# Optimization experiments

Measured on AMD Instinct MI355X. Metric: run time of the kernel, lower is better.

## Reference

```python
import jax, jax.numpy as jnp
import numpy as np
import math

B, N, HW, D, H = 4, 1024, 4096, 512, 8
DK = D // H
EPS = 0.1


def setup_inputs() -> dict:
    key = jax.random.key(0)
    ks = jax.random.split(key, 12)
    s = 1.0 / math.sqrt(D)
    query = jax.random.normal(ks[0], (B, N, D), dtype=jnp.float32)
    key_t = jax.random.normal(ks[1], (B, HW, D), dtype=jnp.float32)
    value = jax.random.normal(ks[2], (B, HW, D), dtype=jnp.float32)
    # 2D spatial positions of the feature map in [0,1]^2
    x_tilde = jax.random.uniform(ks[3], (HW, 2), dtype=jnp.float32)
    # predicted positions per query: close to x_tilde so each row has unmasked keys
    x_hat = x_tilde[None, :, :] + 0.1 * jax.random.normal(ks[4], (N, HW, 2), dtype=jnp.float32)
    Wq = jax.random.normal(ks[5], (D, D), dtype=jnp.float32) * s
    Wk = jax.random.normal(ks[6], (D, D), dtype=jnp.float32) * s
    Wv = jax.random.normal(ks[7], (D, D), dtype=jnp.float32) * s
    Wo = jax.random.normal(ks[8], (D, D), dtype=jnp.float32) * s
    bq = jnp.zeros((D,), jnp.float32)
    bk = jnp.zeros((D,), jnp.float32)
    bv = jnp.zeros((D,), jnp.float32)
    bo = jnp.zeros((D,), jnp.float32)
    return {"query": query, "key": key_t, "value": value,
            "x_tilde": x_tilde, "x_hat": x_hat,
            "Wq": Wq, "bq": bq, "Wk": Wk, "bk": bk,
            "Wv": Wv, "bv": bv, "Wo": Wo, "bo": bo}


def reference(query, key, value, x_tilde, x_hat, Wq, bq, Wk, bk, Wv, bv, Wo, bo):
    b, n, d = query.shape
    hw = key.shape[1]
    # nn.Linear: x @ W^T + b
    Q = (query @ Wq.T + bq).reshape(b, n, H, DK).transpose(0, 2, 1, 3)   # [B,H,N,DK]
    K = (key @ Wk.T + bk).reshape(b, hw, H, DK).transpose(0, 2, 1, 3)    # [B,H,HW,DK]
    V = (value @ Wv.T + bv).reshape(b, hw, H, DK).transpose(0, 2, 1, 3)  # [B,H,HW,DK]
    scores = jnp.einsum('bhnd,bhmd->bhnm', Q, K) / math.sqrt(DK)         # [B,H,N,HW]
    # geometric mask: 0 where ||x_tilde_j - x_hat_ij|| < eps else -inf
    dist = jnp.linalg.norm(x_tilde[None, :, :] - x_hat, axis=-1)         # [N,HW]
    m_geo = jnp.where(dist < EPS, 0.0, -jnp.inf).astype(scores.dtype)
    scores = scores + m_geo[None, None, :, :]
    attn = jax.nn.softmax(scores, axis=-1)                               # [B,H,N,HW]
    # dropout is identity in eval mode
    ctx = jnp.einsum('bhnm,bhmd->bhnd', attn, V)                         # [B,H,N,DK]
    ctx = ctx.transpose(0, 2, 1, 3).reshape(b, n, d)
    out = ctx @ Wo.T + bo
    return (out, attn)
```

## Files before the change

kernel.cpp:

```cpp
#include <hip/hip_runtime.h>
#include <math.h>

typedef _Float16 h8 __attribute__((ext_vector_type(8)));
typedef _Float16 h4 __attribute__((ext_vector_type(4)));
typedef float    f4 __attribute__((ext_vector_type(4)));

#define NQ    1024
#define HWK   4096
#define DM    512
#define NH    8
#define DKH   64

__device__ inline h8 cvt_h8(const float* __restrict__ p) {
    const f4* q = (const f4*)p;
    f4 a = q[0], b = q[1];
    h8 r;
    r[0] = (_Float16)a[0]; r[1] = (_Float16)a[1];
    r[2] = (_Float16)a[2]; r[3] = (_Float16)a[3];
    r[4] = (_Float16)b[0]; r[5] = (_Float16)b[1];
    r[6] = (_Float16)b[2]; r[7] = (_Float16)b[3];
    return r;
}

__global__ __launch_bounds__(256)
void mask_kernel(const float* __restrict__ x_tilde, const float* __restrict__ x_hat,
                 _Float16* __restrict__ maskT)
{
    __shared__ _Float16 T[64][72];
    int t  = threadIdx.x;
    int jl = t & 63;
    int iw = t >> 6;
    int j0 = blockIdx.x * 64;
    int i0 = blockIdx.y * 64;

    float xt0 = x_tilde[(j0 + jl) * 2 + 0];
    float xt1 = x_tilde[(j0 + jl) * 2 + 1];

    for (int ii = iw; ii < 64; ii += 4) {
        size_t idx = ((size_t)(i0 + ii) * HWK + j0 + jl) * 2;
        float h0 = x_hat[idx + 0];
        float h1 = x_hat[idx + 1];
        float dx = xt0 - h0, dy = xt1 - h1;
        float d2 = __fadd_rn(__fmul_rn(dx, dx), __fmul_rn(dy, dy));
        float dist = __fsqrt_rn(d2);
        T[ii][jl] = (dist < 0.1f) ? (_Float16)0.0f : (_Float16)(-__builtin_inff());
    }
    __syncthreads();
    int il = t & 63;
    for (int jj = iw; jj < 64; jj += 4) {
        maskT[(size_t)(j0 + jj) * NQ + i0 + il] = T[il][jj];
    }
}

__global__ __launch_bounds__(256)
void proj_qk(const float* __restrict__ X, const float* __restrict__ W,
             const float* __restrict__ bias, _Float16* __restrict__ out,
             int nlog2, float scale)
{
    int tid = threadIdx.x;
    int w = tid >> 6, lane = tid & 63, q = lane >> 4, c = lane & 15;
    int wr = blockIdx.x * 128 + (w >> 1) * 64;
    int wc = blockIdx.y * 128 + (w & 1) * 64;

    f4 acc[4][4];
    const f4 fz = {0.f, 0.f, 0.f, 0.f};
#pragma unroll
    for (int i = 0; i < 4; i++)
#pragma unroll
        for (int j = 0; j < 4; j++) acc[i][j] = fz;

    for (int k0 = 0; k0 < DM; k0 += 32) {
        h8 af[4], bf[4];
#pragma unroll
        for (int i = 0; i < 4; i++)
            af[i] = cvt_h8(X + (size_t)(wr + i * 16 + c) * DM + k0 + q * 8);
#pragma unroll
        for (int j = 0; j < 4; j++)
            bf[j] = cvt_h8(W + (size_t)(wc + j * 16 + c) * DM + k0 + q * 8);
#pragma unroll
        for (int i = 0; i < 4; i++)
#pragma unroll
            for (int j = 0; j < 4; j++)
                acc[i][j] = __builtin_amdgcn_mfma_f32_16x16x32_f16(af[i], bf[j], acc[i][j], 0, 0, 0);
    }

    int nmask = (1 << nlog2) - 1;
#pragma unroll
    for (int j = 0; j < 4; j++) {
        int ncol = wc + j * 16 + c;
        float bb = bias[ncol];
        int hh = ncol >> 6, dk = ncol & 63;
#pragma unroll
        for (int i = 0; i < 4; i++) {
#pragma unroll
            for (int r = 0; r < 4; r++) {
                int m = wr + i * 16 + q * 4 + r;
                int b = m >> nlog2, n = m & nmask;
                float v = (acc[i][j][r] + bb) * scale;
                out[((((size_t)(b * NH + hh)) << nlog2) + n) * DKH + dk] = (_Float16)v;
            }
        }
    }
}

__global__ __launch_bounds__(256)
void proj_v(const float* __restrict__ V, const float* __restrict__ W,
            const float* __restrict__ bias, _Float16* __restrict__ out)
{
    int tid = threadIdx.x;
    int w = tid >> 6, lane = tid & 63, q = lane >> 4, c = lane & 15;
    int wr = blockIdx.x * 128 + (w >> 1) * 64;
    int wc = blockIdx.y * 128 + (w & 1) * 64;

    f4 acc[4][4];
    const f4 fz = {0.f, 0.f, 0.f, 0.f};
#pragma unroll
    for (int i = 0; i < 4; i++)
#pragma unroll
        for (int j = 0; j < 4; j++) acc[i][j] = fz;

    for (int k0 = 0; k0 < DM; k0 += 32) {
        h8 af[4], bf[4];
#pragma unroll
        for (int i = 0; i < 4; i++)
            af[i] = cvt_h8(W + (size_t)(wr + i * 16 + c) * DM + k0 + q * 8);
#pragma unroll
        for (int j = 0; j < 4; j++)
            bf[j] = cvt_h8(V + (size_t)(wc + j * 16 + c) * DM + k0 + q * 8);
#pragma unroll
        for (int i = 0; i < 4; i++)
#pragma unroll
            for (int j = 0; j < 4; j++)
                acc[i][j] = __builtin_amdgcn_mfma_f32_16x16x32_f16(af[i], bf[j], acc[i][j], 0, 0, 0);
    }

#pragma unroll
    for (int i = 0; i < 4; i++) {
#pragma unroll
        for (int r = 0; r < 4; r++) {
            int f = wr + i * 16 + q * 4 + r;
            float bb = bias[f];
            int hh = f >> 6, dk = f & 63;
#pragma unroll
            for (int j = 0; j < 4; j++) {
                int col = wc + j * 16 + c;
                int b = col >> 12, hw = col & 4095;
                out[((size_t)(b * NH + hh) * DKH + dk) * HWK + hw] =
                    (_Float16)(acc[i][j][r] + bb);
            }
        }
    }
}

__global__ __launch_bounds__(256)
void proj_o(const _Float16* __restrict__ C, const float* __restrict__ W,
            const float* __restrict__ bias, float* __restrict__ out)
{
    int tid = threadIdx.x;
    int w = tid >> 6, lane = tid & 63, q = lane >> 4, c = lane & 15;
    int wr = blockIdx.x * 128 + (w >> 1) * 64;
    int wc = blockIdx.y * 128 + (w & 1) * 64;

    f4 acc[4][4];
    const f4 fz = {0.f, 0.f, 0.f, 0.f};
#pragma unroll
    for (int i = 0; i < 4; i++)
#pragma unroll
        for (int j = 0; j < 4; j++) acc[i][j] = fz;

    for (int k0 = 0; k0 < DM; k0 += 32) {
        h8 af[4], bf[4];
#pragma unroll
        for (int i = 0; i < 4; i++)
            af[i] = *(const h8*)(C + (size_t)(wr + i * 16 + c) * DM + k0 + q * 8);
#pragma unroll
        for (int j = 0; j < 4; j++)
            bf[j] = cvt_h8(W + (size_t)(wc + j * 16 + c) * DM + k0 + q * 8);
#pragma unroll
        for (int i = 0; i < 4; i++)
#pragma unroll
            for (int j = 0; j < 4; j++)
                acc[i][j] = __builtin_amdgcn_mfma_f32_16x16x32_f16(af[i], bf[j], acc[i][j], 0, 0, 0);
    }

#pragma unroll
    for (int j = 0; j < 4; j++) {
        int ncol = wc + j * 16 + c;
        float bb = bias[ncol];
#pragma unroll
        for (int i = 0; i < 4; i++) {
#pragma unroll
            for (int r = 0; r < 4; r++) {
                int m = wr + i * 16 + q * 4 + r;
                out[(size_t)m * DM + ncol] = acc[i][j][r] + bb;
            }
        }
    }
}

__global__ __launch_bounds__(256)
void attn_kernel(const _Float16* __restrict__ Qh, const _Float16* __restrict__ Kh,
                 const _Float16* __restrict__ Vt, const _Float16* __restrict__ maskT,
                 float* __restrict__ attn_out, _Float16* __restrict__ ctx_h)
{
    __shared__ union SmU {
        _Float16 P[4][64][72];
        float    C[64][68];
    } sm;
    __shared__ float red[4][64];
    __shared__ float invl[64];

    int tid = threadIdx.x;
    int w = tid >> 6, lane = tid & 63, q = lane >> 4, c = lane & 15;
    int bh = blockIdx.x >> 4;
    int n0 = (blockIdx.x & 15) * 64;
    int b = bh >> 3, h = bh & 7;

    const _Float16* Qb = Qh + ((size_t)bh * NQ + n0) * DKH;
    const _Float16* Kb = Kh + (size_t)bh * HWK * DKH;
    const _Float16* Vb = Vt + (size_t)bh * DKH * HWK;
    float* attn_b = attn_out + ((size_t)bh * NQ + n0) * HWK;

    h8 qa[4][2];
#pragma unroll
    for (int i = 0; i < 4; i++)
#pragma unroll
        for (int ks = 0; ks < 2; ks++)
            qa[i][ks] = *(const h8*)(Qb + (size_t)(i * 16 + c) * DKH + ks * 32 + q * 8);

    float lsum[4][4];
#pragma unroll
    for (int i = 0; i < 4; i++)
#pragma unroll
        for (int r = 0; r < 4; r++) lsum[i][r] = 0.f;

    for (int it = 0; it < 16; ++it) {
        int m0 = it * 256 + w * 64;
        h8 kb[4][2];
#pragma unroll
        for (int j = 0; j < 4; j++)
#pragma unroll
            for (int ks = 0; ks < 2; ks++)
                kb[j][ks] = *(const h8*)(Kb + (size_t)(m0 + j * 16 + c) * DKH + ks * 32 + q * 8);
#pragma unroll
        for (int i = 0; i < 4; i++) {
#pragma unroll
            for (int j = 0; j < 4; j++) {
                f4 acc = {0.f, 0.f, 0.f, 0.f};
                acc = __builtin_amdgcn_mfma_f32_16x16x32_f16(qa[i][0], kb[j][0], acc, 0, 0, 0);
                acc = __builtin_amdgcn_mfma_f32_16x16x32_f16(qa[i][1], kb[j][1], acc, 0, 0, 0);
                h4 mk = *(const h4*)(maskT + (size_t)(m0 + j * 16 + c) * NQ + n0 + i * 16 + q * 4);
#pragma unroll
                for (int r = 0; r < 4; r++)
                    lsum[i][r] += __expf(acc[r] + (float)mk[r]);
            }
        }
    }

#pragma unroll
    for (int i = 0; i < 4; i++) {
#pragma unroll
        for (int r = 0; r < 4; r++) {
            float s = lsum[i][r];
            s += __shfl_xor(s, 1);
            s += __shfl_xor(s, 2);
            s += __shfl_xor(s, 4);
            s += __shfl_xor(s, 8);
            if (c == 0) red[w][i * 16 + q * 4 + r] = s;
        }
    }
    __syncthreads();
    if (tid < 64)
        invl[tid] = 1.0f / (red[0][tid] + red[1][tid] + red[2][tid] + red[3][tid]);
    __syncthreads();

    f4 cacc[4][4];
    const f4 fz = {0.f, 0.f, 0.f, 0.f};
#pragma unroll
    for (int i = 0; i < 4; i++)
#pragma unroll
        for (int jd = 0; jd < 4; jd++) cacc[i][jd] = fz;

    for (int it = 0; it < 16; ++it) {
        int m0 = it * 256 + w * 64;
        h8 kb[4][2];
#pragma unroll
        for (int j = 0; j < 4; j++)
#pragma unroll
            for (int ks = 0; ks < 2; ks++)
                kb[j][ks] = *(const h8*)(Kb + (size_t)(m0 + j * 16 + c) * DKH + ks * 32 + q * 8);

#pragma unroll
        for (int i = 0; i < 4; i++) {
#pragma unroll
            for (int j = 0; j < 4; j++) {
                f4 acc = {0.f, 0.f, 0.f, 0.f};
                acc = __builtin_amdgcn_mfma_f32_16x16x32_f16(qa[i][0], kb[j][0], acc, 0, 0, 0);
                acc = __builtin_amdgcn_mfma_f32_16x16x32_f16(qa[i][1], kb[j][1], acc, 0, 0, 0);
                h4 mk = *(const h4*)(maskT + (size_t)(m0 + j * 16 + c) * NQ + n0 + i * 16 + q * 4);
#pragma unroll
                for (int r = 0; r < 4; r++) {
                    float e = __expf(acc[r] + (float)mk[r]);
                    sm.P[w][i * 16 + q * 4 + r][j * 16 + c] = (_Float16)e;
                }
            }
        }
#pragma unroll
        for (int ks = 0; ks < 2; ks++) {
            h8 pa[4], vb[4];
#pragma unroll
            for (int i = 0; i < 4; i++)
                pa[i] = *(const h8*)&sm.P[w][i * 16 + c][ks * 32 + q * 8];
#pragma unroll
            for (int jd = 0; jd < 4; jd++)
                vb[jd] = *(const h8*)(Vb + (size_t)(jd * 16 + c) * HWK + m0 + ks * 32 + q * 8);
#pragma unroll
            for (int i = 0; i < 4; i++)
#pragma unroll
                for (int jd = 0; jd < 4; jd++)
                    cacc[i][jd] = __builtin_amdgcn_mfma_f32_16x16x32_f16(pa[i], vb[jd], cacc[i][jd], 0, 0, 0);
        }
#pragma unroll
        for (int r0 = 0; r0 < 64; r0 += 4) {
            int row = r0 + q;
            h4 pv = *(const h4*)&sm.P[w][row][c * 4];
            float il = invl[row];
            f4 o;
            o[0] = (float)pv[0] * il;
            o[1] = (float)pv[1] * il;
            o[2] = (float)pv[2] * il;
            o[3] = (float)pv[3] * il;
            *(f4*)(attn_b + (size_t)row * HWK + m0 + c * 4) = o;
        }
    }

    __syncthreads();
    for (int idx = tid; idx < 64 * 68; idx += 256)
        (&sm.C[0][0])[idx] = 0.f;
    __syncthreads();
#pragma unroll
    for (int i = 0; i < 4; i++)
#pragma unroll
        for (int jd = 0; jd < 4; jd++)
#pragma unroll
            for (int r = 0; r < 4; r++)
                atomicAdd(&sm.C[i * 16 + q * 4 + r][jd * 16 + c], cacc[i][jd][r]);
    __syncthreads();

    _Float16* ctx_b = ctx_h + ((size_t)b * NQ + n0) * DM + h * DKH;
    for (int r0 = 0; r0 < 64; r0 += 4) {
        int row = r0 + w;
        int col = tid & 63;
        float v = sm.C[row][col] * invl[row];
        ctx_b[(size_t)row * DM + col] = (_Float16)v;
    }
}

extern "C" void kernel_launch(void* const* d_in, const int* in_sizes, int n_in,
                              void* d_out, int out_size, void* d_ws, size_t ws_size,
                              hipStream_t stream)
{
    const float* query   = (const float*)d_in[0];
    const float* key     = (const float*)d_in[1];
    const float* value   = (const float*)d_in[2];
    const float* x_tilde = (const float*)d_in[3];
    const float* x_hat   = (const float*)d_in[4];
    const float* Wq = (const float*)d_in[5];
    const float* bq = (const float*)d_in[6];
    const float* Wk = (const float*)d_in[7];
    const float* bk = (const float*)d_in[8];
    const float* Wv = (const float*)d_in[9];
    const float* bv = (const float*)d_in[10];
    const float* Wo = (const float*)d_in[11];
    const float* bo = (const float*)d_in[12];

    char* ws = (char*)d_ws;
    _Float16* Qh    = (_Float16*)(ws);
    _Float16* Kh    = (_Float16*)(ws + ((size_t)4  << 20));
    _Float16* Vt    = (_Float16*)(ws + ((size_t)20 << 20));
    _Float16* ctxh  = (_Float16*)(ws + ((size_t)36 << 20));
    _Float16* maskT = (_Float16*)(ws + ((size_t)40 << 20));

    float* out  = (float*)d_out;
    float* attn = out + (size_t)4 * NQ * DM;

    mask_kernel<<<dim3(HWK / 64, NQ / 64), 256, 0, stream>>>(x_tilde, x_hat, maskT);
    proj_qk<<<dim3(4 * NQ / 128, DM / 128), 256, 0, stream>>>(query, Wq, bq, Qh, 10, 0.125f);
    proj_qk<<<dim3(4 * HWK / 128, DM / 128), 256, 0, stream>>>(key, Wk, bk, Kh, 12, 1.0f);
    proj_v<<<dim3(DM / 128, 4 * HWK / 128), 256, 0, stream>>>(value, Wv, bv, Vt);
    attn_kernel<<<32 * (NQ / 64), 256, 0, stream>>>(Qh, Kh, Vt, maskT, attn, ctxh);
    proj_o<<<dim3(4 * NQ / 128, DM / 128), 256, 0, stream>>>(ctxh, Wo, bo, out);
}
```

Baseline: 1.039 ms.

## Split attention into score/exp kernel and PV kernel with materialized fp16 exp buffer

Replaces the fused two-pass attention kernel, which computed QK^T twice, with one kernel that computes exp(scores+mask) once. That kernel writes the values to an fp16 global buffer and atomically accumulates row sums. A second kernel reads the buffer to do the PV matmul and write the normalized attention output. The mask is now stored untransposed in row order, and the recompute of the score matmul is removed. In exchange it adds a 268MB fp16 write and reads it back twice, plus an extra memset and launch.

Measured after the change: 1.240 ms. 1.19x slower.

```diff
diff --git a/kernel.cpp b/kernel.cpp
--- a/kernel.cpp
+++ b/kernel.cpp
@@ -24,32 +24,19 @@
 
 __global__ __launch_bounds__(256)
 void mask_kernel(const float* __restrict__ x_tilde, const float* __restrict__ x_hat,
-                 _Float16* __restrict__ maskT)
-{
-    __shared__ _Float16 T[64][72];
-    int t  = threadIdx.x;
-    int jl = t & 63;
-    int iw = t >> 6;
-    int j0 = blockIdx.x * 64;
-    int i0 = blockIdx.y * 64;
-
-    float xt0 = x_tilde[(j0 + jl) * 2 + 0];
-    float xt1 = x_tilde[(j0 + jl) * 2 + 1];
-
-    for (int ii = iw; ii < 64; ii += 4) {
-        size_t idx = ((size_t)(i0 + ii) * HWK + j0 + jl) * 2;
-        float h0 = x_hat[idx + 0];
-        float h1 = x_hat[idx + 1];
-        float dx = xt0 - h0, dy = xt1 - h1;
-        float d2 = __fadd_rn(__fmul_rn(dx, dx), __fmul_rn(dy, dy));
-        float dist = __fsqrt_rn(d2);
-        T[ii][jl] = (dist < 0.1f) ? (_Float16)0.0f : (_Float16)(-__builtin_inff());
-    }
-    __syncthreads();
-    int il = t & 63;
-    for (int jj = iw; jj < 64; jj += 4) {
-        maskT[(size_t)(j0 + jj) * NQ + i0 + il] = T[il][jj];
-    }
+                 _Float16* __restrict__ mask)
+{
+    int hw = blockIdx.x * 256 + threadIdx.x;
+    int n  = blockIdx.y;
+    float xt0 = x_tilde[hw * 2 + 0];
+    float xt1 = x_tilde[hw * 2 + 1];
+    size_t idx = ((size_t)n * HWK + hw) * 2;
+    float dx = xt0 - x_hat[idx + 0];
+    float dy = xt1 - x_hat[idx + 1];
+    float d2 = __fadd_rn(__fmul_rn(dx, dx), __fmul_rn(dy, dy));
+    float dist = __fsqrt_rn(d2);
+    mask[(size_t)n * HWK + hw] = (dist < 0.1f) ? (_Float16)0.0f
+                                               : (_Float16)(-__builtin_inff());
 }
 
 __global__ __launch_bounds__(256)
@@ -199,160 +186,147 @@
 }
 
 __global__ __launch_bounds__(256)
-void attn_kernel(const _Float16* __restrict__ Qh, const _Float16* __restrict__ Kh,
-                 const _Float16* __restrict__ Vt, const _Float16* __restrict__ maskT,
-                 float* __restrict__ attn_out, _Float16* __restrict__ ctx_h)
-{
-    __shared__ union SmU {
-        _Float16 P[4][64][72];
-        float    C[64][68];
-    } sm;
+void attn_scores(const _Float16* __restrict__ Qh, const _Float16* __restrict__ Kh,
+                 const _Float16* __restrict__ mask,
+                 _Float16* __restrict__ eBuf, float* __restrict__ lsum_g)
+{
     __shared__ float red[4][64];
-    __shared__ float invl[64];
-
-    int tid = threadIdx.x;
-    int w = tid >> 6, lane = tid & 63, q = lane >> 4, c = lane & 15;
-    int bh = blockIdx.x >> 4;
-    int n0 = (blockIdx.x & 15) * 64;
-    int b = bh >> 3, h = bh & 7;
+    int tid = threadIdx.x;
+    int w = tid >> 6, lane = tid & 63, q = lane >> 4, c = lane & 15;
+    int bx = blockIdx.x;
+    int mt = bx & 3, nt = (bx >> 2) & 15, bh = bx >> 6;
+    int n0 = nt * 64;
 
     const _Float16* Qb = Qh + ((size_t)bh * NQ + n0) * DKH;
     const _Float16* Kb = Kh + (size_t)bh * HWK * DKH;
+    _Float16* eb = eBuf + (size_t)bh * NQ * HWK;
+
+    h8 qb[4][2];
+#pragma unroll
+    for (int j = 0; j < 4; j++)
+#pragma unroll
+        for (int ks = 0; ks < 2; ks++)
+            qb[j][ks] = *(const h8*)(Qb + (size_t)(j * 16 + c) * DKH + ks * 32 + q * 8);
+
+    float lsum[4] = {0.f, 0.f, 0.f, 0.f};
+
+    for (int it = 0; it < 4; ++it) {
+        int m0 = mt * 1024 + w * 256 + it * 64;
+        h8 ka[4][2];
+#pragma unroll
+        for (int i = 0; i < 4; i++)
+#pragma unroll
+            for (int ks = 0; ks < 2; ks++)
+                ka[i][ks] = *(const h8*)(Kb + (size_t)(m0 + i * 16 + c) * DKH + ks * 32 + q * 8);
+
+#pragma unroll
+        for (int i = 0; i < 4; i++) {
+#pragma unroll
+            for (int j = 0; j < 4; j++) {
+                f4 acc = {0.f, 0.f, 0.f, 0.f};
+                acc = __builtin_amdgcn_mfma_f32_16x16x32_f16(ka[i][0], qb[j][0], acc, 0, 0, 0);
+                acc = __builtin_amdgcn_mfma_f32_16x16x32_f16(ka[i][1], qb[j][1], acc, 0, 0, 0);
+                size_t roff = (size_t)(n0 + j * 16 + c) * HWK + m0 + i * 16 + q * 4;
+                h4 mk = *(const h4*)(mask + roff);
+                h4 ev;
+#pragma unroll
+                for (int r = 0; r < 4; r++) {
+                    float e = __expf(acc[r] + (float)mk[r]);
+                    lsum[j] += e;
+                    ev[r] = (_Float16)e;
+                }
+                *(h4*)(eb + roff) = ev;
+            }
+        }
+    }
+
+#pragma unroll
+    for (int j = 0; j < 4; j++) {
+        float s = lsum[j];
+        s += __shfl_xor(s, 16);
+        s += __shfl_xor(s, 32);
+        if (q == 0) red[w][j * 16 + c] = s;
+    }
+    __syncthreads();
+    if (tid < 64)
+        atomicAdd(lsum_g + (size_t)bh * NQ + n0 + tid,
+                  red[0][tid] + red[1][tid] + red[2][tid] + red[3][tid]);
+}
+
+__global__ __launch_bounds__(256)
+void attn_pv(const _Float16* __restrict__ eBuf, const _Float16* __restrict__ Vt,
+             const float* __restrict__ lsum_g,
+             float* __restrict__ attn_out, _Float16* __restrict__ ctx_h)
+{
+    __shared__ float invS[16];
+    __shared__ float Cr[16][68];
+
+    int tid = threadIdx.x;
+    int w = tid >> 6, lane = tid & 63, q = lane >> 4, c = lane & 15;
+    int nt = blockIdx.x & 63, bh = blockIdx.x >> 6;
+    int n0 = nt * 16;
+
+    if (tid < 16) invS[tid] = 1.0f / lsum_g[(size_t)bh * NQ + n0 + tid];
+    for (int idx = tid; idx < 16 * 68; idx += 256) (&Cr[0][0])[idx] = 0.f;
+    __syncthreads();
+
+    const _Float16* eb = eBuf + ((size_t)bh * NQ + n0) * HWK;
     const _Float16* Vb = Vt + (size_t)bh * DKH * HWK;
-    float* attn_b = attn_out + ((size_t)bh * NQ + n0) * HWK;
-
-    h8 qa[4][2];
-#pragma unroll
-    for (int i = 0; i < 4; i++)
-#pragma unroll
-        for (int ks = 0; ks < 2; ks++)
-            qa[i][ks] = *(const h8*)(Qb + (size_t)(i * 16 + c) * DKH + ks * 32 + q * 8);
-
-    float lsum[4][4];
-#pragma unroll
-    for (int i = 0; i < 4; i++)
-#pragma unroll
-        for (int r = 0; r < 4; r++) lsum[i][r] = 0.f;
+    float* ab = attn_out + ((size_t)bh * NQ + n0) * HWK;
+
+    f4 cacc[4];
+    const f4 fz = {0.f, 0.f, 0.f, 0.f};
+#pragma unroll
+    for (int jd = 0; jd < 4; jd++) cacc[jd] = fz;
 
     for (int it = 0; it < 16; ++it) {
         int m0 = it * 256 + w * 64;
-        h8 kb[4][2];
-#pragma unroll
-        for (int j = 0; j < 4; j++)
+        h8 pa[2];
+#pragma unroll
+        for (int ks = 0; ks < 2; ks++)
+            pa[ks] = *(const h8*)(eb + (size_t)c * HWK + m0 + ks * 32 + q * 8);
+        h8 vb[4][2];
+#pragma unroll
+        for (int jd = 0; jd < 4; jd++)
 #pragma unroll
             for (int ks = 0; ks < 2; ks++)
-                kb[j][ks] = *(const h8*)(Kb + (size_t)(m0 + j * 16 + c) * DKH + ks * 32 + q * 8);
-#pragma unroll
-        for (int i = 0; i < 4; i++) {
-#pragma unroll
-            for (int j = 0; j < 4; j++) {
-                f4 acc = {0.f, 0.f, 0.f, 0.f};
-                acc = __builtin_amdgcn_mfma_f32_16x16x32_f16(qa[i][0], kb[j][0], acc, 0, 0, 0);
-                acc = __builtin_amdgcn_mfma_f32_16x16x32_f16(qa[i][1], kb[j][1], acc, 0, 0, 0);
-                h4 mk = *(const h4*)(maskT + (size_t)(m0 + j * 16 + c) * NQ + n0 + i * 16 + q * 4);
-#pragma unroll
-                for (int r = 0; r < 4; r++)
-                    lsum[i][r] += __expf(acc[r] + (float)mk[r]);
-            }
-        }
-    }
-
-#pragma unroll
-    for (int i = 0; i < 4; i++) {
-#pragma unroll
-        for (int r = 0; r < 4; r++) {
-            float s = lsum[i][r];
-            s += __shfl_xor(s, 1);
-            s += __shfl_xor(s, 2);
-            s += __shfl_xor(s, 4);
-            s += __shfl_xor(s, 8);
-            if (c == 0) red[w][i * 16 + q * 4 + r] = s;
-        }
-    }
+                vb[jd][ks] = *(const h8*)(Vb + (size_t)(jd * 16 + c) * HWK + m0 + ks * 32 + q * 8);
+#pragma unroll
+        for (int jd = 0; jd < 4; jd++) {
+            cacc[jd] = __builtin_amdgcn_mfma_f32_16x16x32_f16(pa[0], vb[jd][0], cacc[jd], 0, 0, 0);
+            cacc[jd] = __builtin_amdgcn_mfma_f32_16x16x32_f16(pa[1], vb[jd][1], cacc[jd], 0, 0, 0);
+        }
+#pragma unroll
+        for (int s = 0; s < 2; s++) {
+            int row = s * 8 + (lane >> 3);
+            int mc = (lane & 7) * 8;
+            h8 e8 = *(const h8*)(eb + (size_t)row * HWK + m0 + mc);
+            float il = invS[row];
+            f4 o0, o1;
+            o0[0] = (float)e8[0] * il; o0[1] = (float)e8[1] * il;
+            o0[2] = (float)e8[2] * il; o0[3] = (float)e8[3] * il;
+            o1[0] = (float)e8[4] * il; o1[1] = (float)e8[5] * il;
+            o1[2] = (float)e8[6] * il; o1[3] = (float)e8[7] * il;
+            float* dst = ab + (size_t)row * HWK + m0 + mc;
+            *(f4*)dst = o0;
+            *(f4*)(dst + 4) = o1;
+        }
+    }
+
+#pragma unroll
+    for (int jd = 0; jd < 4; jd++)
+#pragma unroll
+        for (int r = 0; r < 4; r++)
+            atomicAdd(&Cr[q * 4 + r][jd * 16 + c], cacc[jd][r]);
     __syncthreads();
-    if (tid < 64)
-        invl[tid] = 1.0f / (red[0][tid] + red[1][tid] + red[2][tid] + red[3][tid]);
-    __syncthreads();
-
-    f4 cacc[4][4];
-    const f4 fz = {0.f, 0.f, 0.f, 0.f};
-#pragma unroll
-    for (int i = 0; i < 4; i++)
-#pragma unroll
-        for (int jd = 0; jd < 4; jd++) cacc[i][jd] = fz;
-
-    for (int it = 0; it < 16; ++it) {
-        int m0 = it * 256 + w * 64;
-        h8 kb[4][2];
-#pragma unroll
-        for (int j = 0; j < 4; j++)
-#pragma unroll
-            for (int ks = 0; ks < 2; ks++)
-                kb[j][ks] = *(const h8*)(Kb + (size_t)(m0 + j * 16 + c) * DKH + ks * 32 + q * 8);
-
-#pragma unroll
-        for (int i = 0; i < 4; i++) {
-#pragma unroll
-            for (int j = 0; j < 4; j++) {
-                f4 acc = {0.f, 0.f, 0.f, 0.f};
-                acc = __builtin_amdgcn_mfma_f32_16x16x32_f16(qa[i][0], kb[j][0], acc, 0, 0, 0);
-                acc = __builtin_amdgcn_mfma_f32_16x16x32_f16(qa[i][1], kb[j][1], acc, 0, 0, 0);
-                h4 mk = *(const h4*)(maskT + (size_t)(m0 + j * 16 + c) * NQ + n0 + i * 16 + q * 4);
-#pragma unroll
-                for (int r = 0; r < 4; r++) {
-                    float e = __expf(acc[r] + (float)mk[r]);
-                    sm.P[w][i * 16 + q * 4 + r][j * 16 + c] = (_Float16)e;
-                }
-            }
-        }
-#pragma unroll
-        for (int ks = 0; ks < 2; ks++) {
-            h8 pa[4], vb[4];
-#pragma unroll
-            for (int i = 0; i < 4; i++)
-                pa[i] = *(const h8*)&sm.P[w][i * 16 + c][ks * 32 + q * 8];
-#pragma unroll
-            for (int jd = 0; jd < 4; jd++)
-                vb[jd] = *(const h8*)(Vb + (size_t)(jd * 16 + c) * HWK + m0 + ks * 32 + q * 8);
-#pragma unroll
-            for (int i = 0; i < 4; i++)
-#pragma unroll
-                for (int jd = 0; jd < 4; jd++)
-                    cacc[i][jd] = __builtin_amdgcn_mfma_f32_16x16x32_f16(pa[i], vb[jd], cacc[i][jd], 0, 0, 0);
-        }
-#pragma unroll
-        for (int r0 = 0; r0 < 64; r0 += 4) {
-            int row = r0 + q;
-            h4 pv = *(const h4*)&sm.P[w][row][c * 4];
-            float il = invl[row];
-            f4 o;
-            o[0] = (float)pv[0] * il;
-            o[1] = (float)pv[1] * il;
-            o[2] = (float)pv[2] * il;
-            o[3] = (float)pv[3] * il;
-            *(f4*)(attn_b + (size_t)row * HWK + m0 + c * 4) = o;
-        }
-    }
-
-    __syncthreads();
-    for (int idx = tid; idx < 64 * 68; idx += 256)
-        (&sm.C[0][0])[idx] = 0.f;
-    __syncthreads();
-#pragma unroll
-    for (int i = 0; i < 4; i++)
-#pragma unroll
-        for (int jd = 0; jd < 4; jd++)
-#pragma unroll
-            for (int r = 0; r < 4; r++)
-                atomicAdd(&sm.C[i * 16 + q * 4 + r][jd * 16 + c], cacc[i][jd][r]);
-    __syncthreads();
-
-    _Float16* ctx_b = ctx_h + ((size_t)b * NQ + n0) * DM + h * DKH;
-    for (int r0 = 0; r0 < 64; r0 += 4) {
-        int row = r0 + w;
+
+    int b = bh >> 3, h = bh & 7;
+    _Float16* cb = ctx_h + ((size_t)b * NQ + n0) * DM + h * DKH;
+#pragma unroll
+    for (int g = 0; g < 4; g++) {
+        int row = g * 4 + (tid >> 6);
         int col = tid & 63;
-        float v = sm.C[row][col] * invl[row];
-        ctx_b[(size_t)row * DM + col] = (_Float16)v;
+        cb[(size_t)row * DM + col] = (_Float16)(Cr[row][col] * invS[row]);
     }
 }
 
@@ -379,15 +353,20 @@
     _Float16* Kh    = (_Float16*)(ws + ((size_t)4  << 20));
     _Float16* Vt    = (_Float16*)(ws + ((size_t)20 << 20));
     _Float16* ctxh  = (_Float16*)(ws + ((size_t)36 << 20));
-    _Float16* maskT = (_Float16*)(ws + ((size_t)40 << 20));
+    _Float16* mask  = (_Float16*)(ws + ((size_t)40 << 20));
+    float*    lsum  = (float*)   (ws + ((size_t)48 << 20));
+    _Float16* eBuf  = (_Float16*)(ws + ((size_t)52 << 20));
 
     float* out  = (float*)d_out;
     float* attn = out + (size_t)4 * NQ * DM;
 
-    mask_kernel<<<dim3(HWK / 64, NQ / 64), 256, 0, stream>>>(x_tilde, x_hat, maskT);
+    hipMemsetAsync(lsum, 0, (size_t)4 * NH * NQ * sizeof(float), stream);
+
+    mask_kernel<<<dim3(HWK / 256, NQ), 256, 0, stream>>>(x_tilde, x_hat, mask);
     proj_qk<<<dim3(4 * NQ / 128, DM / 128), 256, 0, stream>>>(query, Wq, bq, Qh, 10, 0.125f);
     proj_qk<<<dim3(4 * HWK / 128, DM / 128), 256, 0, stream>>>(key, Wk, bk, Kh, 12, 1.0f);
     proj_v<<<dim3(DM / 128, 4 * HWK / 128), 256, 0, stream>>>(value, Wv, bv, Vt);
-    attn_kernel<<<32 * (NQ / 64), 256, 0, stream>>>(Qh, Kh, Vt, maskT, attn, ctxh);
+    attn_scores<<<32 * 16 * 4, 256, 0, stream>>>(Qh, Kh, mask, eBuf, lsum);
+    attn_pv<<<32 * 64, 256, 0, stream>>>(eBuf, Vt, lsum, attn, ctxh);
     proj_o<<<dim3(4 * NQ / 128, DM / 128), 256, 0, stream>>>(ctxh, Wo, bo, out);
 }
```
